# Optimization experiments

Measured on AMD Instinct MI355X. Metric: run time of the kernel, lower is better.

The kernel has to match this reference:

```python
import jax, jax.numpy as jnp
import numpy as np
from jax import lax

B, T, P, I, H = 1024, 100, 50, 96, 1024  # batch, seq_dim, pred_dim, input_dim, hidden_dim


def _gru_cell(x, h, Wih, Whh, bih, bhh):
    # PyTorch GRU gate math. Wih:[3H,in], Whh:[3H,H]
    gi = x @ Wih.T + bih
    gh = h @ Whh.T + bhh
    ir, iz, i_n = jnp.split(gi, 3, axis=-1)
    hr, hz, h_n = jnp.split(gh, 3, axis=-1)
    r = jax.nn.sigmoid(ir + hr)
    z = jax.nn.sigmoid(iz + hz)
    n = jnp.tanh(i_n + r * h_n)
    return (1.0 - z) * n + z * h


def setup_inputs() -> dict:
    key = jax.random.key(0)
    ks = jax.random.split(key, 24)
    s = 1.0 / np.sqrt(H)

    def rn(k, shape):
        return jax.random.normal(k, shape, jnp.float32) * s

    inp = {"x": jax.random.normal(ks[0], (B, T, I), jnp.float32)}
    # encoder nn.GRU: layer 0 input I, layer 1 input H
    inp["enc_Wih0"] = rn(ks[1], (3 * H, I)); inp["enc_Whh0"] = rn(ks[2], (3 * H, H))
    inp["enc_bih0"] = rn(ks[3], (3 * H,));   inp["enc_bhh0"] = rn(ks[4], (3 * H,))
    inp["enc_Wih1"] = rn(ks[5], (3 * H, H)); inp["enc_Whh1"] = rn(ks[6], (3 * H, H))
    inp["enc_bih1"] = rn(ks[7], (3 * H,));   inp["enc_bhh1"] = rn(ks[8], (3 * H,))
    # decoder GRUCells (hidden->hidden)
    inp["dec_Wih0"] = rn(ks[9], (3 * H, H)); inp["dec_Whh0"] = rn(ks[10], (3 * H, H))
    inp["dec_bih0"] = rn(ks[11], (3 * H,));  inp["dec_bhh0"] = rn(ks[12], (3 * H,))
    inp["dec_Wih1"] = rn(ks[13], (3 * H, H)); inp["dec_Whh1"] = rn(ks[14], (3 * H, H))
    inp["dec_bih1"] = rn(ks[15], (3 * H,));  inp["dec_bhh1"] = rn(ks[16], (3 * H,))
    # fc_in: I->H, fc_out: H->I
    inp["fc_in_w"] = rn(ks[17], (H, I)); inp["fc_in_b"] = rn(ks[18], (H,))
    inp["fc_out_w"] = rn(ks[19], (I, H)); inp["fc_out_b"] = rn(ks[20], (I,))
    return inp


def reference(x, enc_Wih0, enc_Whh0, enc_bih0, enc_bhh0,
              enc_Wih1, enc_Whh1, enc_bih1, enc_bhh1,
              dec_Wih0, dec_Whh0, dec_bih0, dec_bhh0,
              dec_Wih1, dec_Whh1, dec_bih1, dec_bhh1,
              fc_in_w, fc_in_b, fc_out_w, fc_out_b):
    b = x.shape[0]
    h0 = jnp.zeros((b, H), x.dtype)
    xs = jnp.transpose(x[:, :P, :], (1, 0, 2))  # [P, B, I]

    def enc0(h, xt):
        h2 = _gru_cell(xt, h, enc_Wih0, enc_Whh0, enc_bih0, enc_bhh0)
        return h2, h2

    h_enc0, seq0 = lax.scan(enc0, h0, xs)

    def enc1(h, xt):
        h2 = _gru_cell(xt, h, enc_Wih1, enc_Whh1, enc_bih1, enc_bhh1)
        return h2, h2

    h_enc1, _ = lax.scan(enc1, h0, seq0)

    def dec_step(carry, _):
        frame, hd0, hd1 = carry
        y = frame @ fc_in_w.T + fc_in_b
        hd0 = _gru_cell(y, hd0, dec_Wih0, dec_Whh0, dec_bih0, dec_bhh0)
        hd1 = _gru_cell(hd0, hd1, dec_Wih1, dec_Whh1, dec_bih1, dec_bhh1)
        frame = hd1 @ fc_out_w.T + fc_out_b + frame
        return (frame, hd0, hd1), frame

    init = (x[:, P - 1, :], h_enc0, h_enc1)
    _, outs = lax.scan(dec_step, init, None, length=T - P)  # [T-P, B, I]
    out = jnp.concatenate([x[:, :P, :], jnp.transpose(outs, (1, 0, 2))], axis=1)
    return out
```

## Files before the change

### kernel.cpp

```cpp
#include <hip/hip_runtime.h>
#include <hip/hip_bf16.h>
#include <stdint.h>

#define Bsz 1024
#define Tt  100
#define Pp  50
#define Ii  96
#define Hh  1024
#define H3  3072

typedef __bf16 bf16x8 __attribute__((ext_vector_type(8)));
typedef float f32x4 __attribute__((ext_vector_type(4)));
typedef __hip_bfloat16 bf16;

__device__ __forceinline__ void llds16(const void* g, void* l) {
    __builtin_amdgcn_global_load_lds(
        (const __attribute__((address_space(1))) void*)g,
        (__attribute__((address_space(3))) void*)l,
        16, 0, 0);
}

__device__ __forceinline__ f32x4 ldb4(const bf16* p) {
    ushort4 u = *(const ushort4*)p;
    union { unsigned int i; float f; } c;
    f32x4 r;
    c.i = (unsigned int)u.x << 16; r[0] = c.f;
    c.i = (unsigned int)u.y << 16; r[1] = c.f;
    c.i = (unsigned int)u.z << 16; r[2] = c.f;
    c.i = (unsigned int)u.w << 16; r[3] = c.f;
    return r;
}

__device__ __forceinline__ void swz_decomp(int& bx, int& by, int& bz) {
    int gx = gridDim.x, gy = gridDim.y, gz = gridDim.z;
    int flat = blockIdx.x + gx * (blockIdx.y + gy * blockIdx.z);
    int tot = gx * gy * gz;
    if (!(tot & 7)) {
        int q = tot >> 3;
        flat = (flat & 7) * q + (flat >> 3);
    }
    bx = flat % gx;
    int rest = flat / gx;
    by = rest % gy;
    bz = rest / gy;
}

__global__ void wdesc_k(unsigned long long* slot, const void* A, const void* W,
                        const void* b, void* C, int K, int lda) {
    if (threadIdx.x == 0) {
        slot[0] = (unsigned long long)A;
        slot[1] = (unsigned long long)W;
        slot[2] = (unsigned long long)b;
        slot[3] = (unsigned long long)C;
        slot[4] = (unsigned long long)K;
        slot[5] = (unsigned long long)lda;
    }
}

__global__ void __launch_bounds__(256)
gemm_tab(const unsigned long long* __restrict__ tab, int base, int ndesc,
         const bf16* __restrict__ extraA)
{
    __shared__ bf16 As[128 * 64];
    __shared__ bf16 Ws[128 * 64];
    int flat = blockIdx.x;
    const int tot = ndesc * 192;
    if (!(tot & 7)) {
        int q = tot >> 3;
        flat = (flat & 7) * q + (flat >> 3);
    }
    const int g = flat / 192;
    const int local = flat - g * 192;
    const unsigned long long* dp = tab + (size_t)(base + g) * 8;
    const bf16* A = (const bf16*)dp[0];
    const bf16* W = (const bf16*)dp[1];
    const float* bias = (const float*)dp[2];
    bf16* C = (bf16*)dp[3];
    const int K = (int)dp[4];
    const int lda = (int)dp[5];
    if (!A) A = extraA;

    const int tn = (local % 24) * 128;
    const int tm = (local / 24) * 128;

    const int tid = threadIdx.x;
    const int lane = tid & 63;
    const int wid = tid >> 6;
    const int wr = (wid >> 1) * 64;
    const int wc = (wid & 1) * 64;
    const int srow = tid >> 3;
    const int schk = ((tid & 7) ^ (srow & 7)) * 8;
    const int sdst = tid * 16;
    const int fr = lane & 15;
    const int hi = lane >> 4;

    f32x4 acc[4][4] = {};

    const bf16* ga = A + (size_t)(tm + srow) * lda + schk;
    const bf16* gw = W + (size_t)(tn + srow) * K + schk;
    char* lA = (char*)As + sdst;
    char* lW = (char*)Ws + sdst;
    const int nk = K >> 6;

    for (int kt = 0; kt < nk; ++kt) {
#pragma unroll
        for (int m = 0; m < 4; ++m) {
            llds16(ga + (size_t)(32 * m) * lda, lA + 32 * m * 128);
            llds16(gw + (size_t)(32 * m) * K,  lW + 32 * m * 128);
        }
        ga += 64; gw += 64;
        __syncthreads();

#pragma unroll
        for (int kk = 0; kk < 2; ++kk) {
            bf16x8 af[4], wf[4];
            const int chk = (((kk << 2) + hi) ^ (fr & 7)) * 8;
#pragma unroll
            for (int i = 0; i < 4; ++i) {
                af[i] = *(const bf16x8*)&As[(wr + i * 16 + fr) * 64 + chk];
                wf[i] = *(const bf16x8*)&Ws[(wc + i * 16 + fr) * 64 + chk];
            }
#pragma unroll
            for (int mi = 0; mi < 4; ++mi)
#pragma unroll
                for (int ni = 0; ni < 4; ++ni)
                    acc[mi][ni] = __builtin_amdgcn_mfma_f32_16x16x32_bf16(
                        af[mi], wf[ni], acc[mi][ni], 0, 0, 0);
        }
        __syncthreads();
    }

    const int fq = hi * 4;
#pragma unroll
    for (int mi = 0; mi < 4; ++mi)
#pragma unroll
        for (int ni = 0; ni < 4; ++ni) {
            const int col = tn + wc + ni * 16 + fr;
            const float bv = bias[col];
#pragma unroll
            for (int r = 0; r < 4; ++r) {
                const int row = tm + wr + mi * 16 + fq + r;
                C[(size_t)row * H3 + col] = __float2bfloat16(acc[mi][ni][r] + bv);
            }
        }
}

__global__ void __launch_bounds__(256)
fuse_fg_k(const float* __restrict__ gp,
          const float* __restrict__ fin,
          float* __restrict__ fout,
          float* __restrict__ out_t,
          const bf16* __restrict__ W,
          const float* __restrict__ bias,
          bf16* __restrict__ C)
{
    __shared__ bf16 Af[64 * 136];
    __shared__ bf16 Ws[128 * 64];
    int flat = blockIdx.x;
    { int q = 384 >> 3; flat = (flat & 7) * q + (flat >> 3); }
    const int tn = (flat % 24) * 128;
    const int tm = (flat / 24) * 64;
    const int tid = threadIdx.x;

#pragma unroll
    for (int i = 0; i < 6; ++i) {
        int v = i * 256 + tid;
        int row = v / 24;
        int c4 = (v % 24) * 4;
        size_t go = (size_t)(tm + row) * Ii + c4;
        f32x4 s = {};
#pragma unroll
        for (int p = 0; p < 8; ++p)
            s += *(const f32x4*)(gp + (size_t)p * (Bsz * Ii) + go);
        f32x4 fv = *(const f32x4*)(fin + go) + s;
        if (tn == 0) {
            *(f32x4*)(fout + go) = fv;
            *(f32x4*)(out_t + (size_t)(tm + row) * (Tt * Ii) + c4) = fv;
        }
        ushort4 up;
        unsigned short* us = &up.x;
#pragma unroll
        for (int e = 0; e < 4; ++e) {
            bf16 bv = __float2bfloat16(fv[e]);
            us[e] = *(unsigned short*)&bv;
        }
        *(ushort4*)&Af[row * 136 + c4] = up;
    }
#pragma unroll
    for (int i = 0; i < 2; ++i) {
        int v = i * 256 + tid;
        int row = v >> 3;
        int c4 = 96 + (v & 7) * 4;
        ushort4 z; z.x = 0; z.y = 0; z.z = 0; z.w = 0;
        *(ushort4*)&Af[row * 136 + c4] = z;
    }

    const int lane = tid & 63;
    const int wid = tid >> 6;
    const int wr = (wid >> 1) * 32;
    const int wc = (wid & 1) * 64;
    const int srow = tid >> 3;
    const int schk = ((tid & 7) ^ (srow & 7)) * 8;
    const int sdst = tid * 16;
    const int fr = lane & 15;
    const int hi = lane >> 4;

    f32x4 acc[2][4] = {};
    const bf16* gw = W + (size_t)(tn + srow) * 128 + schk;
    char* lW = (char*)Ws + sdst;

    for (int kt = 0; kt < 2; ++kt) {
#pragma unroll
        for (int m = 0; m < 4; ++m)
            llds16(gw + (size_t)(32 * m) * 128, lW + 32 * m * 128);
        gw += 64;
        __syncthreads();
#pragma unroll
        for (int kk = 0; kk < 2; ++kk) {
            bf16x8 af[2], wf[4];
            const int wchk = (((kk << 2) + hi) ^ (fr & 7)) * 8;
            const int achk = kt * 64 + ((kk << 2) + hi) * 8;
#pragma unroll
            for (int i = 0; i < 2; ++i)
                af[i] = *(const bf16x8*)&Af[(wr + i * 16 + fr) * 136 + achk];
#pragma unroll
            for (int i = 0; i < 4; ++i)
                wf[i] = *(const bf16x8*)&Ws[(wc + i * 16 + fr) * 64 + wchk];
#pragma unroll
            for (int mi = 0; mi < 2; ++mi)
#pragma unroll
                for (int ni = 0; ni < 4; ++ni)
                    acc[mi][ni] = __builtin_amdgcn_mfma_f32_16x16x32_bf16(
                        af[mi], wf[ni], acc[mi][ni], 0, 0, 0);
        }
        __syncthreads();
    }

    const int fq = hi * 4;
#pragma unroll
    for (int mi = 0; mi < 2; ++mi)
#pragma unroll
        for (int ni = 0; ni < 4; ++ni) {
            const int col = tn + wc + ni * 16 + fr;
            const float bv = bias[col];
#pragma unroll
            for (int r = 0; r < 4; ++r) {
                const int row = tm + wr + mi * 16 + fq + r;
                C[(size_t)row * H3 + col] = __float2bfloat16(acc[mi][ni][r] + bv);
            }
        }
}

template <bool OUT_BF16>
__global__ void __launch_bounds__(256)
gemm64(const bf16* __restrict__ A, const bf16* __restrict__ W,
       const float* __restrict__ bias, void* __restrict__ Cout,
       int M, int Nreal, int Ktot, int Ks, int lda, int ldc)
{
    __shared__ bf16 As[64 * 32];
    __shared__ bf16 Ws[64 * 32];
    int bx, by, bz;
    swz_decomp(bx, by, bz);
    const int s = bz;
    const float* bs = (s == 0) ? bias : nullptr;
    const int tid = threadIdx.x;
    const int lane = tid & 63;
    const int wid = tid >> 6;
    const int wr = (wid >> 1) * 32;
    const int wc = (wid & 1) * 32;
    const int tm = by * 64;
    const int tn = bx * 64;
    const int srow = tid >> 2;
    const int skb = (tid & 3) * 8;
    const int k0 = s * Ks;

    f32x4 acc[2][2] = {};

    const bf16* ga = A + (size_t)(tm + srow) * lda + k0 + skb;
    const bf16* gw = W + (size_t)(tn + srow) * Ktot + k0 + skb;
    bf16* lA = &As[srow * 32 + skb];
    bf16* lW = &Ws[srow * 32 + skb];
    const int nk = Ks >> 5;

    for (int kt = 0; kt < nk; ++kt) {
        llds16(ga, lA);
        llds16(gw, lW);
        ga += 32; gw += 32;
        __syncthreads();
        const int fr = lane & 15;
        const int kg = (lane >> 4) * 8;
        bf16x8 af[2], wf[2];
#pragma unroll
        for (int i = 0; i < 2; ++i) {
            af[i] = *(const bf16x8*)&As[(wr + i * 16 + fr) * 32 + kg];
            wf[i] = *(const bf16x8*)&Ws[(wc + i * 16 + fr) * 32 + kg];
        }
#pragma unroll
        for (int mi = 0; mi < 2; ++mi)
#pragma unroll
            for (int ni = 0; ni < 2; ++ni)
                acc[mi][ni] = __builtin_amdgcn_mfma_f32_16x16x32_bf16(
                    af[mi], wf[ni], acc[mi][ni], 0, 0, 0);
        __syncthreads();
    }

    float* Cf = (float*)Cout + (size_t)s * M * ldc;
    const int fr = lane & 15;
    const int fq = (lane >> 4) * 4;
#pragma unroll
    for (int mi = 0; mi < 2; ++mi)
#pragma unroll
        for (int ni = 0; ni < 2; ++ni) {
            const int col = tn + wc + ni * 16 + fr;
            if (col < Nreal) {
                const float bv = bs ? bs[col] : 0.f;
#pragma unroll
                for (int r = 0; r < 4; ++r) {
                    const int row = tm + wr + mi * 16 + fq + r;
                    const float v = acc[mi][ni][r] + bv;
                    if constexpr (OUT_BF16)
                        ((bf16*)Cout)[(size_t)row * ldc + col] = __float2bfloat16(v);
                    else
                        Cf[(size_t)row * ldc + col] = v;
                }
            }
        }
}

__global__ void cvt_k(const float* __restrict__ s, bf16* __restrict__ d, int n) {
    int i = blockIdx.x * blockDim.x + threadIdx.x;
    if (i < n) d[i] = __float2bfloat16(s[i]);
}

__global__ void cvtpad_k(const float* __restrict__ s, bf16* __restrict__ d, int n) {
    int o = blockIdx.x * blockDim.x + threadIdx.x;
    if (o >= n * 128) return;
    int r = o >> 7, c = o & 127;
    d[o] = __float2bfloat16(c < Ii ? s[(size_t)r * Ii + c] : 0.f);
}

__global__ void tpose_k(const float* __restrict__ x, bf16* __restrict__ d) {
    int o = blockIdx.x * blockDim.x + threadIdx.x;
    if (o >= Tt * Bsz * 128) return;
    int i = o & 127;
    int b = (o >> 7) & (Bsz - 1);
    int t = o >> 17;
    d[o] = __float2bfloat16(i < Ii ? x[((size_t)b * Tt + t) * Ii + i] : 0.f);
}

__global__ void tposeFcin_k(const float* __restrict__ w, bf16* __restrict__ d) {
    int o = blockIdx.x * blockDim.x + threadIdx.x;
    if (o >= 128 * Hh) return;
    int r = o >> 10;
    int c = o & (Hh - 1);
    float v = (r < Ii) ? w[(size_t)c * Ii + r] : 0.f;
    d[o] = __float2bfloat16(v);
}

__global__ void __launch_bounds__(256)
bcomb_k(const float* __restrict__ W, const float* __restrict__ v,
        const float* __restrict__ b2, float* __restrict__ o) {
    __shared__ float red[256];
    int n = blockIdx.x;
    float s = 0.f;
    for (int k = threadIdx.x; k < Hh; k += 256)
        s += W[(size_t)n * Hh + k] * v[k];
    red[threadIdx.x] = s;
    __syncthreads();
    for (int w = 128; w > 0; w >>= 1) {
        if (threadIdx.x < w) red[threadIdx.x] += red[threadIdx.x + w];
        __syncthreads();
    }
    if (threadIdx.x == 0) o[n] = red[0] + b2[n];
}

__global__ void prefix_k(const float* __restrict__ x, float* __restrict__ out) {
    int idx = blockIdx.x * blockDim.x + threadIdx.x;
    if (idx >= Bsz * Pp * Ii) return;
    int b = idx / (Pp * Ii);
    int r = idx % (Pp * Ii);
    out[(size_t)b * Tt * Ii + r] = x[(size_t)b * Tt * Ii + r];
}

__global__ void finit_k(const float* __restrict__ x, float* __restrict__ fr,
                        bf16* __restrict__ frb) {
    int idx = blockIdx.x * blockDim.x + threadIdx.x;
    if (idx >= Bsz * Ii) return;
    int b = idx / Ii;
    int i = idx % Ii;
    float v = x[(size_t)b * Tt * Ii + (Pp - 1) * Ii + i];
    fr[idx] = v;
    frb[(size_t)b * 128 + i] = __float2bfloat16(v);
}

#define CELL_BODY(IDX, GI, GH, H, HB)                                        \
    {                                                                        \
        int b_ = (IDX) >> 8;                                                 \
        int j_ = ((IDX) & 255) << 2;                                         \
        size_t base_ = (size_t)b_ * H3 + j_;                                 \
        f32x4 ir = ldb4((GI) + base_);                                       \
        f32x4 iz = ldb4((GI) + base_ + Hh);                                  \
        f32x4 in = ldb4((GI) + base_ + 2 * Hh);                              \
        f32x4 hr = ldb4((GH) + base_);                                       \
        f32x4 hz = ldb4((GH) + base_ + Hh);                                  \
        f32x4 hn = ldb4((GH) + base_ + 2 * Hh);                              \
        size_t hoff_ = (size_t)b_ * Hh + j_;                                 \
        f32x4 hold = *(const f32x4*)((H) + hoff_);                           \
        f32x4 hv;                                                            \
        ushort4 up;                                                          \
        unsigned short* us = &up.x;                                          \
        _Pragma("unroll")                                                    \
        for (int e = 0; e < 4; ++e) {                                        \
            float r = 1.f / (1.f + __expf(-(ir[e] + hr[e])));                \
            float z = 1.f / (1.f + __expf(-(iz[e] + hz[e])));                \
            float n = tanhf(in[e] + r * hn[e]);                              \
            float v = (1.f - z) * n + z * hold[e];                           \
            hv[e] = v;                                                       \
            bf16 bv = __float2bfloat16(v);                                   \
            us[e] = *(unsigned short*)&bv;                                   \
        }                                                                    \
        *(f32x4*)((H) + hoff_) = hv;                                         \
        *(ushort4*)((unsigned short*)(HB) + hoff_) = up;                     \
    }

__global__ void __launch_bounds__(256)
gru_cell_k(const bf16* __restrict__ gi, const bf16* __restrict__ gh,
           float* __restrict__ h, bf16* __restrict__ hb) {
    int idx = blockIdx.x * 256 + threadIdx.x;
    CELL_BODY(idx, gi, gh, h, hb);
}

__global__ void __launch_bounds__(256)
gru_cell2_k(const bf16* __restrict__ giA, const bf16* __restrict__ ghA,
            float* __restrict__ hA, bf16* __restrict__ hbA,
            const bf16* __restrict__ giB, const bf16* __restrict__ ghB,
            float* __restrict__ hB, bf16* __restrict__ hbB) {
    int bid = blockIdx.x;
    const bf16* gi = giA;
    const bf16* gh = ghA;
    float* h = hA;
    bf16* hb = hbA;
    if (bid >= 1024) {
        gi = giB; gh = ghB; h = hB; hb = hbB;
        bid -= 1024;
    }
    int idx = bid * 256 + threadIdx.x;
    CELL_BODY(idx, gi, gh, h, hb);
}

extern "C" void kernel_launch(void* const* d_in, const int* in_sizes, int n_in,
                              void* d_out, int out_size, void* d_ws, size_t ws_size,
                              hipStream_t stream) {
    const float* x      = (const float*)d_in[0];
    const float* eWih0  = (const float*)d_in[1];
    const float* eWhh0  = (const float*)d_in[2];
    const float* ebih0  = (const float*)d_in[3];
    const float* ebhh0  = (const float*)d_in[4];
    const float* eWih1  = (const float*)d_in[5];
    const float* eWhh1  = (const float*)d_in[6];
    const float* ebih1  = (const float*)d_in[7];
    const float* ebhh1  = (const float*)d_in[8];
    const float* dWih0  = (const float*)d_in[9];
    const float* dWhh0  = (const float*)d_in[10];
    const float* dbih0  = (const float*)d_in[11];
    const float* dbhh0  = (const float*)d_in[12];
    const float* dWih1  = (const float*)d_in[13];
    const float* dWhh1  = (const float*)d_in[14];
    const float* dbih1  = (const float*)d_in[15];
    const float* dbhh1  = (const float*)d_in[16];
    const float* fcin_w = (const float*)d_in[17];
    const float* fcin_b = (const float*)d_in[18];
    const float* fcout_w= (const float*)d_in[19];
    const float* fcout_b= (const float*)d_in[20];
    float* out = (float*)d_out;

    char* base = (char*)d_ws;
    size_t off = 0;
    auto alloc = [&](size_t bytes) -> void* {
        void* r = base + off;
        off += (bytes + 255) & ~(size_t)255;
        return r;
    };
    bf16* wWih0e = (bf16*)alloc((size_t)H3 * 128 * 2);
    bf16* wWhh0e = (bf16*)alloc((size_t)H3 * Hh * 2);
    bf16* wWih1e = (bf16*)alloc((size_t)H3 * Hh * 2);
    bf16* wWhh1e = (bf16*)alloc((size_t)H3 * Hh * 2);
    bf16* wWhh0d = (bf16*)alloc((size_t)H3 * Hh * 2);
    bf16* wWih1d = (bf16*)alloc((size_t)H3 * Hh * 2);
    bf16* wWhh1d = (bf16*)alloc((size_t)H3 * Hh * 2);
    bf16* wWih0d = (bf16*)alloc((size_t)H3 * Hh * 2);
    bf16* fcinT  = (bf16*)alloc((size_t)128 * Hh * 2);
    bf16* wWcomb = (bf16*)alloc((size_t)H3 * 128 * 2);
    float* bcomb = (float*)alloc((size_t)H3 * 4);
    bf16* wfcout = (bf16*)alloc((size_t)128 * Hh * 2);
    float* zbias = (float*)alloc((size_t)128 * 4);
    bf16* xbT    = (bf16*)alloc((size_t)Tt * Bsz * 128 * 2);
    bf16* gi1_p  = (bf16*)alloc((size_t)Bsz * H3 * 2);
    bf16* gh1_p  = (bf16*)alloc((size_t)Bsz * H3 * 2);
    bf16* gh0_p  = (bf16*)alloc((size_t)Bsz * H3 * 2);
    bf16* gi0_p  = (bf16*)alloc((size_t)Bsz * H3 * 2);
    float* h0    = (float*)alloc((size_t)Bsz * Hh * 4);
    float* h1    = (float*)alloc((size_t)Bsz * Hh * 4);
    bf16* h0b    = (bf16*)alloc((size_t)Bsz * Hh * 2);
    bf16* h1b    = (bf16*)alloc((size_t)Bsz * Hh * 2);
    float* gfc   = (float*)alloc((size_t)8 * Bsz * Ii * 4);
    float* fbuf0 = (float*)alloc((size_t)Bsz * Ii * 4);
    float* fbuf1 = (float*)alloc((size_t)Bsz * Ii * 4);
    bf16* frameb = (bf16*)alloc((size_t)Bsz * 128 * 2);
    unsigned long long* tab = (unsigned long long*)alloc(8 * 8 * 8);
    if (off > ws_size) return;

    auto cvt = [&](const float* s, bf16* d, int n) {
        cvt_k<<<dim3((n + 255) / 256), dim3(256), 0, stream>>>(s, d, n);
    };
    cvtpad_k<<<dim3((H3 * 128 + 255) / 256), dim3(256), 0, stream>>>(eWih0, wWih0e, H3);
    cvt(eWhh0, wWhh0e, H3 * Hh);
    cvt(eWih1, wWih1e, H3 * Hh);
    cvt(eWhh1, wWhh1e, H3 * Hh);
    cvt(dWih0, wWih0d, H3 * Hh);
    cvt(dWhh0, wWhh0d, H3 * Hh);
    cvt(dWih1, wWih1d, H3 * Hh);
    cvt(dWhh1, wWhh1d, H3 * Hh);
    (void)hipMemsetAsync(wfcout, 0, (size_t)128 * Hh * 2, stream);
    (void)hipMemsetAsync(wWcomb, 0, (size_t)H3 * 128 * 2, stream);
    (void)hipMemsetAsync(zbias, 0, (size_t)128 * 4, stream);
    (void)hipMemsetAsync(frameb, 0, (size_t)Bsz * 128 * 2, stream);
    cvt(fcout_w, wfcout, Ii * Hh);
    tposeFcin_k<<<dim3((128 * Hh + 255) / 256), dim3(256), 0, stream>>>(fcin_w, fcinT);
    gemm64<true><<<dim3(2, 48, 1), dim3(256), 0, stream>>>(
        wWih0d, fcinT, zbias, (void*)wWcomb, H3, Ii, Hh, Hh, Hh, 128);
    bcomb_k<<<dim3(H3), dim3(256), 0, stream>>>(dWih0, fcin_b, dbih0, bcomb);

    tpose_k<<<dim3((Tt * Bsz * 128 + 255) / 256), dim3(256), 0, stream>>>(x, xbT);
    prefix_k<<<dim3((Bsz * Pp * Ii + 255) / 256), dim3(256), 0, stream>>>(x, out);
    finit_k<<<dim3((Bsz * Ii + 255) / 256), dim3(256), 0, stream>>>(x, fbuf0, frameb);
    (void)hipMemsetAsync(h0, 0, (size_t)Bsz * Hh * 4, stream);
    (void)hipMemsetAsync(h1, 0, (size_t)Bsz * Hh * 4, stream);
    (void)hipMemsetAsync(h0b, 0, (size_t)Bsz * Hh * 2, stream);
    (void)hipMemsetAsync(h1b, 0, (size_t)Bsz * Hh * 2, stream);

    wdesc_k<<<1, 64, 0, stream>>>(tab + 0 * 8, h0b, wWih1e, ebih1, gi1_p, Hh, Hh);
    wdesc_k<<<1, 64, 0, stream>>>(tab + 1 * 8, h1b, wWhh1e, ebhh1, gh1_p, Hh, Hh);
    wdesc_k<<<1, 64, 0, stream>>>(tab + 2 * 8, h0b, wWhh0e, ebhh0, gh0_p, Hh, Hh);
    wdesc_k<<<1, 64, 0, stream>>>(tab + 3 * 8, nullptr, wWih0e, ebih0, gi0_p, 128, 128);
    wdesc_k<<<1, 64, 0, stream>>>(tab + 4 * 8, h0b, wWih1d, dbih1, gi1_p, Hh, Hh);
    wdesc_k<<<1, 64, 0, stream>>>(tab + 5 * 8, h1b, wWhh1d, dbhh1, gh1_p, Hh, Hh);
    wdesc_k<<<1, 64, 0, stream>>>(tab + 6 * 8, h0b, wWhh0d, dbhh0, gh0_p, Hh, Hh);
    wdesc_k<<<1, 64, 0, stream>>>(tab + 7 * 8, frameb, wWcomb, bcomb, gi0_p, 128, 128);

    gemm_tab<<<dim3(384), dim3(256), 0, stream>>>(tab, 2, 2, xbT);
    gru_cell_k<<<dim3(1024), dim3(256), 0, stream>>>(gi0_p, gh0_p, h0, h0b);
    for (int i = 0; i < Pp; ++i) {
        if (i < Pp - 1) {
            gemm_tab<<<dim3(768), dim3(256), 0, stream>>>(
                tab, 0, 4, xbT + (size_t)(i + 1) * Bsz * 128);
            gru_cell2_k<<<dim3(2048), dim3(256), 0, stream>>>(
                gi1_p, gh1_p, h1, h1b, gi0_p, gh0_p, h0, h0b);
        } else {
            gemm_tab<<<dim3(384), dim3(256), 0, stream>>>(tab, 0, 2, xbT);
            gru_cell_k<<<dim3(1024), dim3(256), 0, stream>>>(gi1_p, gh1_p, h1, h1b);
        }
    }

    gemm_tab<<<dim3(384), dim3(256), 0, stream>>>(tab, 6, 2, xbT);
    gru_cell_k<<<dim3(1024), dim3(256), 0, stream>>>(gi0_p, gh0_p, h0, h0b);
    for (int t = 0; t < Tt - Pp; ++t) {
        const bool last = (t == Tt - Pp - 1);
        if (!last) {
            gemm_tab<<<dim3(576), dim3(256), 0, stream>>>(tab, 4, 3, xbT);
        } else {
            gemm_tab<<<dim3(384), dim3(256), 0, stream>>>(tab, 4, 2, xbT);
        }
        gru_cell_k<<<dim3(1024), dim3(256), 0, stream>>>(gi1_p, gh1_p, h1, h1b);
        gemm64<false><<<dim3(2, 16, 8), dim3(256), 0, stream>>>(
            h1b, wfcout, fcout_b, (void*)gfc, Bsz, Ii, Hh, Hh / 8, Hh, Ii);
        fuse_fg_k<<<dim3(384), dim3(256), 0, stream>>>(
            gfc, (t & 1) ? fbuf1 : fbuf0, (t & 1) ? fbuf0 : fbuf1,
            out + (size_t)(Pp + t) * Ii, wWcomb, bcomb, gi0_p);
        if (!last) {
            gru_cell_k<<<dim3(1024), dim3(256), 0, stream>>>(gi0_p, gh0_p, h0, h0b);
        }
    }
}
```

Measured before the change: 4.936 ms.

## Batch encoder layer-0 input projections across timesteps into chunked precompute GEMMs

The encoder layer-0 input GEMM (x_t @ Wih0) does not depend on the recurrence. It is now computed for up to 10 timesteps at once in a chunked buffer held in spare workspace, instead of being fused into each per-step gemm_tab launch. Per-step launches drop from 4 to 3 descriptors, and the batched launches give larger grids and reuse the weight tile. The cost is extra workspace memory and traffic for the chunk buffers, with a fallback to the old path when the workspace is too small.

```diff
diff --git a/kernel.cpp b/kernel.cpp
--- a/kernel.cpp
+++ b/kernel.cpp
@@ -55,6 +55,19 @@
         slot[4] = (unsigned long long)K;
         slot[5] = (unsigned long long)lda;
     }
+}
+
+__global__ void wdesc_gi0_k(unsigned long long* tab8, const bf16* xbT,
+                            const bf16* W, const float* b, bf16* buf, int CH) {
+    int t = threadIdx.x;
+    if (t >= Pp) return;
+    unsigned long long* slot = tab8 + (size_t)t * 8;
+    slot[0] = (unsigned long long)(xbT + (size_t)t * Bsz * 128);
+    slot[1] = (unsigned long long)W;
+    slot[2] = (unsigned long long)b;
+    slot[3] = (unsigned long long)(buf + (size_t)(t % CH) * Bsz * H3);
+    slot[4] = 128;
+    slot[5] = 128;
 }
 
 __global__ void __launch_bounds__(256)
@@ -507,8 +520,22 @@
     float* fbuf0 = (float*)alloc((size_t)Bsz * Ii * 4);
     float* fbuf1 = (float*)alloc((size_t)Bsz * Ii * 4);
     bf16* frameb = (bf16*)alloc((size_t)Bsz * 128 * 2);
-    unsigned long long* tab = (unsigned long long*)alloc(8 * 8 * 8);
+    unsigned long long* tab = (unsigned long long*)alloc((8 + Pp) * 8 * 8);
     if (off > ws_size) return;
+
+    const size_t PARTb = (size_t)Bsz * H3;
+    int CH = 0;
+    bf16* gi0buf = nullptr;
+    {
+        size_t room = ws_size - off;
+        size_t per = PARTb * 2 + 256;
+        int c = (int)(room / per);
+        if (c > 10) c = 10;
+        if (c >= 2) {
+            CH = c;
+            gi0buf = (bf16*)alloc(PARTb * (size_t)CH * 2);
+        }
+    }
 
     auto cvt = [&](const float* s, bf16* d, int n) {
         cvt_k<<<dim3((n + 255) / 256), dim3(256), 0, stream>>>(s, d, n);
@@ -547,18 +574,44 @@
     wdesc_k<<<1, 64, 0, stream>>>(tab + 5 * 8, h1b, wWhh1d, dbhh1, gh1_p, Hh, Hh);
     wdesc_k<<<1, 64, 0, stream>>>(tab + 6 * 8, h0b, wWhh0d, dbhh0, gh0_p, Hh, Hh);
     wdesc_k<<<1, 64, 0, stream>>>(tab + 7 * 8, frameb, wWcomb, bcomb, gi0_p, 128, 128);
-
-    gemm_tab<<<dim3(384), dim3(256), 0, stream>>>(tab, 2, 2, xbT);
-    gru_cell_k<<<dim3(1024), dim3(256), 0, stream>>>(gi0_p, gh0_p, h0, h0b);
-    for (int i = 0; i < Pp; ++i) {
-        if (i < Pp - 1) {
-            gemm_tab<<<dim3(768), dim3(256), 0, stream>>>(
-                tab, 0, 4, xbT + (size_t)(i + 1) * Bsz * 128);
-            gru_cell2_k<<<dim3(2048), dim3(256), 0, stream>>>(
-                gi1_p, gh1_p, h1, h1b, gi0_p, gh0_p, h0, h0b);
-        } else {
-            gemm_tab<<<dim3(384), dim3(256), 0, stream>>>(tab, 0, 2, xbT);
-            gru_cell_k<<<dim3(1024), dim3(256), 0, stream>>>(gi1_p, gh1_p, h1, h1b);
+    if (CH)
+        wdesc_gi0_k<<<1, 64, 0, stream>>>(tab + 8 * 8, xbT, wWih0e, ebih0, gi0buf, CH);
+
+    if (CH) {
+        int len0 = (Pp < CH) ? Pp : CH;
+        gemm_tab<<<dim3(len0 * 192), dim3(256), 0, stream>>>(tab, 8, len0, xbT);
+        gemm_tab<<<dim3(192), dim3(256), 0, stream>>>(tab, 2, 1, xbT);
+        gru_cell_k<<<dim3(1024), dim3(256), 0, stream>>>(gi0buf, gh0_p, h0, h0b);
+        for (int i = 0; i < Pp; ++i) {
+            if ((i + 1) < Pp && ((i + 1) % CH) == 0) {
+                int t0 = i + 1;
+                int len = (Pp - t0 < CH) ? (Pp - t0) : CH;
+                gemm_tab<<<dim3(len * 192), dim3(256), 0, stream>>>(
+                    tab, 8 + t0, len, xbT);
+            }
+            if (i < Pp - 1) {
+                gemm_tab<<<dim3(576), dim3(256), 0, stream>>>(tab, 0, 3, xbT);
+                gru_cell2_k<<<dim3(2048), dim3(256), 0, stream>>>(
+                    gi1_p, gh1_p, h1, h1b,
+                    gi0buf + (size_t)((i + 1) % CH) * PARTb, gh0_p, h0, h0b);
+            } else {
+                gemm_tab<<<dim3(384), dim3(256), 0, stream>>>(tab, 0, 2, xbT);
+                gru_cell_k<<<dim3(1024), dim3(256), 0, stream>>>(gi1_p, gh1_p, h1, h1b);
+            }
+        }
+    } else {
+        gemm_tab<<<dim3(384), dim3(256), 0, stream>>>(tab, 2, 2, xbT);
+        gru_cell_k<<<dim3(1024), dim3(256), 0, stream>>>(gi0_p, gh0_p, h0, h0b);
+        for (int i = 0; i < Pp; ++i) {
+            if (i < Pp - 1) {
+                gemm_tab<<<dim3(768), dim3(256), 0, stream>>>(
+                    tab, 0, 4, xbT + (size_t)(i + 1) * Bsz * 128);
+                gru_cell2_k<<<dim3(2048), dim3(256), 0, stream>>>(
+                    gi1_p, gh1_p, h1, h1b, gi0_p, gh0_p, h0, h0b);
+            } else {
+                gemm_tab<<<dim3(384), dim3(256), 0, stream>>>(tab, 0, 2, xbT);
+                gru_cell_k<<<dim3(1024), dim3(256), 0, stream>>>(gi1_p, gh1_p, h1, h1b);
+            }
         }
     }
 
```

Measured after the change: 5.112 ms. 1.04x slower.
